# Performance work log

Hardware: AMD Instinct MI355X
Metric: run time of the kernel (lower is better)

Reference implementation:

```python
import jax, jax.numpy as jnp
import numpy as np

N_NODES = 100000
N_EDGES = 3200000
N_GRAPHS = 64
DIMS = [512, 1024, 512, 256, 128, 64, 32]
N_CLASSES = 10


def setup_inputs() -> dict:
    key = jax.random.key(0)
    ks = jax.random.split(key, 20)
    inp = {}
    inp['h'] = jax.random.normal(ks[0], (N_NODES, DIMS[0]), dtype=jnp.float32)
    inp['src'] = jax.random.randint(ks[1], (N_EDGES,), 0, N_NODES, dtype=jnp.int32)
    inp['dst'] = jax.random.randint(ks[2], (N_EDGES,), 0, N_NODES, dtype=jnp.int32)
    inp['graph_ids'] = jnp.sort(jax.random.randint(ks[3], (N_NODES,), 0, N_GRAPHS, dtype=jnp.int32))
    # GraphConv weights (glorot-like) and biases for the 6 layers
    for i in range(6):
        fi, fo = DIMS[i], DIMS[i + 1]
        scale = jnp.sqrt(2.0 / (fi + fo)).astype(jnp.float32)
        inp[f'W{i+1}'] = jax.random.normal(ks[4 + i], (fi, fo), dtype=jnp.float32) * scale
        inp[f'b{i+1}'] = jnp.zeros((fo,), dtype=jnp.float32)
    inp['Wc'] = jax.random.normal(ks[12], (DIMS[-1], N_CLASSES), dtype=jnp.float32) * 0.1
    inp['bc'] = jnp.zeros((N_CLASSES,), dtype=jnp.float32)
    return inp


def _graph_conv(h, W, b, src, dst, out_inv_sqrt, in_inv_sqrt):
    """DGL GraphConv, norm='both': D_dst^{-1/2} A (D_src^{-1/2} h) W + b.
    Apply W first when it shrinks the feature dim (DGL's mult-first trick)."""
    fi, fo = W.shape
    if fi > fo:
        h = h @ W  # shrink before aggregating
    h = h * out_inv_sqrt[:, None]
    agg = jax.ops.segment_sum(h[src], dst, num_segments=N_NODES)  # SpMM
    agg = agg * in_inv_sqrt[:, None]
    if fi <= fo:
        agg = agg @ W
    return agg + b


def reference(h, src, dst, graph_ids, W1, b1, W2, b2, W3, b3, W4, b4, W5, b5, W6, b6, Wc, bc):
    ones_e = jnp.ones((N_EDGES,), dtype=jnp.float32)
    out_deg = jax.ops.segment_sum(ones_e, src, num_segments=N_NODES)
    in_deg = jax.ops.segment_sum(ones_e, dst, num_segments=N_NODES)
    out_inv_sqrt = jax.lax.rsqrt(jnp.clip(out_deg, 1.0))  # allow_zero_in_degree -> clamp
    in_inv_sqrt = jax.lax.rsqrt(jnp.clip(in_deg, 1.0))
    for (W, b) in [(W1, b1), (W2, b2), (W3, b3), (W4, b4), (W5, b5), (W6, b6)]:
        h = jax.nn.relu(_graph_conv(h, W, b, src, dst, out_inv_sqrt, in_inv_sqrt))
    # dgl.mean_nodes over batched graph
    sums = jax.ops.segment_sum(h, graph_ids, num_segments=N_GRAPHS)
    counts = jax.ops.segment_sum(jnp.ones((N_NODES,), jnp.float32), graph_ids, num_segments=N_GRAPHS)
    hg = sums / jnp.clip(counts, 1.0)[:, None]
    return hg @ Wc + bc  # [N_GRAPHS, n_classes]
```

## Files before the change

### kernel.cpp

```cpp
#include <hip/hip_runtime.h>

#define N_NODES 100000
#define N_EDGES 3200000
#define N_GRAPHS 64

typedef unsigned short u16;
typedef __bf16 bf16x8 __attribute__((ext_vector_type(8)));
typedef float f32x4 __attribute__((ext_vector_type(4)));

__device__ inline u16 f2bf(float f) {
  unsigned u = __float_as_uint(f);
  unsigned r = (u + 0x7fffu + ((u >> 16) & 1u)) >> 16;
  return (u16)r;
}
__device__ inline float bf2f(u16 h) {
  return __uint_as_float(((unsigned)h) << 16);
}

__global__ void k_hist(const int* __restrict__ src, const int* __restrict__ dst,
                       int* __restrict__ odeg, int* __restrict__ ideg) {
  int e = blockIdx.x * blockDim.x + threadIdx.x;
  if (e < N_EDGES) {
    atomicAdd(&odeg[src[e]], 1);
    atomicAdd(&ideg[dst[e]], 1);
  }
}

__global__ void k_scan_block(const int* __restrict__ deg, int* __restrict__ rp,
                             int* __restrict__ bsums) {
  __shared__ int s[1024];
  int t = threadIdx.x;
  int i = blockIdx.x * 1024 + t;
  int v = (i < N_NODES) ? deg[i] : 0;
  s[t] = v;
  __syncthreads();
  for (int off = 1; off < 1024; off <<= 1) {
    int add = (t >= off) ? s[t - off] : 0;
    __syncthreads();
    s[t] += add;
    __syncthreads();
  }
  if (i < N_NODES) rp[i + 1] = s[t];
  if (t == 1023) bsums[blockIdx.x] = s[t];
  if (i == 0) rp[0] = 0;
}

__global__ void k_scan_bsums(int* __restrict__ bsums, int nb) {
  __shared__ int s[128];
  int t = threadIdx.x;
  int v = (t < nb) ? bsums[t] : 0;
  s[t] = v;
  __syncthreads();
  for (int off = 1; off < 128; off <<= 1) {
    int add = (t >= off) ? s[t - off] : 0;
    __syncthreads();
    s[t] += add;
    __syncthreads();
  }
  if (t < nb) bsums[t] = s[t];
}

__global__ void k_scan_add(const int* __restrict__ bsums, int* __restrict__ rp) {
  int b = blockIdx.x;
  if (b == 0) return;
  int i = b * 1024 + threadIdx.x;
  if (i < N_NODES) rp[i + 1] += bsums[b - 1];
}

__global__ void k_scatter(const int* __restrict__ src, const int* __restrict__ dst,
                          const int* __restrict__ rp, int* __restrict__ cur,
                          int* __restrict__ col) {
  int e = blockIdx.x * blockDim.x + threadIdx.x;
  if (e < N_EDGES) {
    int d = dst[e];
    int pos = rp[d] + atomicAdd(&cur[d], 1);
    col[pos] = src[e];
  }
}

__global__ void k_rsqrt(const int* __restrict__ odeg, const int* __restrict__ ideg,
                        float* __restrict__ a, float* __restrict__ bI) {
  int v = blockIdx.x * blockDim.x + threadIdx.x;
  if (v < N_NODES) {
    a[v]  = rsqrtf(fmaxf((float)odeg[v], 1.0f));
    bI[v] = rsqrtf(fmaxf((float)ideg[v], 1.0f));
  }
}

__global__ void k_f2bf(const float* __restrict__ x, u16* __restrict__ y, int n4) {
  int i = blockIdx.x * blockDim.x + threadIdx.x;
  if (i >= n4) return;
  float4 v = ((const float4*)x)[i];
  uint2 o;
  o.x = (unsigned)f2bf(v.x) | ((unsigned)f2bf(v.y) << 16);
  o.y = (unsigned)f2bf(v.z) | ((unsigned)f2bf(v.w) << 16);
  ((uint2*)y)[i] = o;
}

__global__ void k_wt(const float* __restrict__ W, u16* __restrict__ Wt, int fi, int fo) {
  int idx = blockIdx.x * blockDim.x + threadIdx.x;
  if (idx >= fi * fo) return;
  int n = idx / fi, k = idx % fi;
  Wt[idx] = f2bf(W[(size_t)k * fo + n]);
}

template<int BM, int BN, int WM, int WN>
__global__ __launch_bounds__(256) void k_mfma(
    const u16* __restrict__ A, const u16* __restrict__ Wt,
    const float* __restrict__ bias, const float* __restrict__ rowscale,
    u16* __restrict__ C, int M, int N, int K, int flags)
{
  constexpr int BK = 32;
  constexpr int LDK = BK + 8;
  constexpr int WX = BN / WN;
  constexpr int WY = BM / WM;
  static_assert(WX * WY == 4, "4 waves");
  constexpr int TM = WM / 16;
  constexpr int TN = WN / 16;

  __shared__ u16 As[BM * LDK];
  __shared__ u16 Bs[BN * LDK];

  const int tid = threadIdx.x;
  const int wave = tid >> 6;
  const int lane = tid & 63;
  const int wx = wave % WX;
  const int wy = wave / WX;
  const int bm = blockIdx.y * BM;
  const int bn = blockIdx.x * BN;

  const int lm = lane & 15;
  const int kb = (lane >> 4) * 8;

  f32x4 acc[TM][TN] = {};

  for (int k0 = 0; k0 < K; k0 += BK) {
    for (int idx = tid; idx < BM * 4; idx += 256) {
      int r = idx >> 2, kk = (idx & 3) * 8;
      int row = bm + r;
      uint4 v = make_uint4(0, 0, 0, 0);
      if (row < M) v = *(const uint4*)(A + (size_t)row * K + k0 + kk);
      *(uint4*)&As[r * LDK + kk] = v;
    }
    for (int idx = tid; idx < BN * 4; idx += 256) {
      int r = idx >> 2, kk = (idx & 3) * 8;
      *(uint4*)&Bs[r * LDK + kk] = *(const uint4*)(Wt + (size_t)(bn + r) * K + k0 + kk);
    }
    __syncthreads();

    bf16x8 af[TM], bfr[TN];
    #pragma unroll
    for (int i = 0; i < TM; ++i)
      af[i] = *(const bf16x8*)&As[(wy * WM + i * 16 + lm) * LDK + kb];
    #pragma unroll
    for (int j = 0; j < TN; ++j)
      bfr[j] = *(const bf16x8*)&Bs[(wx * WN + j * 16 + lm) * LDK + kb];
    #pragma unroll
    for (int i = 0; i < TM; ++i)
      #pragma unroll
      for (int j = 0; j < TN; ++j)
        acc[i][j] = __builtin_amdgcn_mfma_f32_16x16x32_bf16(af[i], bfr[j], acc[i][j], 0, 0, 0);
    __syncthreads();
  }

  const bool do_br = flags & 1;
  const bool do_rs = flags & 2;
  #pragma unroll
  for (int i = 0; i < TM; ++i) {
    #pragma unroll
    for (int j = 0; j < TN; ++j) {
      int col = bn + wx * WN + j * 16 + lm;
      float bv = do_br ? bias[col] : 0.f;
      #pragma unroll
      for (int r = 0; r < 4; ++r) {
        int row = bm + wy * WM + i * 16 + (lane >> 4) * 4 + r;
        if (row < M) {
          float v = acc[i][j][r];
          if (do_rs) v *= rowscale[row];
          if (do_br) v = fmaxf(v + bv, 0.f);
          C[(size_t)row * N + col] = f2bf(v);
        }
      }
    }
  }
}

template<int D>
__global__ __launch_bounds__(256) void k_spmm(
    const int* __restrict__ rp, const int* __restrict__ col,
    const u16* __restrict__ X, const float* __restrict__ sscale,
    const float* __restrict__ dscale, const float* __restrict__ bias,
    u16* __restrict__ Y, int relu_bias)
{
  constexpr int TPR = D / 8;
  constexpr int NPB = 256 / TPR;
  int node = blockIdx.x * NPB + threadIdx.x / TPR;
  if (node >= N_NODES) return;
  int c = (threadIdx.x % TPR) * 8;
  int s = rp[node], e = rp[node + 1];
  float acc[8] = {};
  for (int j = s; j < e; ++j) {
    int u = col[j];
    float w = sscale ? sscale[u] : 1.0f;
    uint4 v = *(const uint4*)(X + (size_t)u * D + c);
    acc[0] += w * __uint_as_float(v.x << 16);
    acc[1] += w * __uint_as_float(v.x & 0xffff0000u);
    acc[2] += w * __uint_as_float(v.y << 16);
    acc[3] += w * __uint_as_float(v.y & 0xffff0000u);
    acc[4] += w * __uint_as_float(v.z << 16);
    acc[5] += w * __uint_as_float(v.z & 0xffff0000u);
    acc[6] += w * __uint_as_float(v.w << 16);
    acc[7] += w * __uint_as_float(v.w & 0xffff0000u);
  }
  float dv = dscale[node];
  #pragma unroll
  for (int q = 0; q < 8; ++q) acc[q] *= dv;
  if (relu_bias) {
    #pragma unroll
    for (int q = 0; q < 8; ++q) acc[q] = fmaxf(acc[q] + bias[c + q], 0.f);
  }
  uint4 o;
  o.x = (unsigned)f2bf(acc[0]) | ((unsigned)f2bf(acc[1]) << 16);
  o.y = (unsigned)f2bf(acc[2]) | ((unsigned)f2bf(acc[3]) << 16);
  o.z = (unsigned)f2bf(acc[4]) | ((unsigned)f2bf(acc[5]) << 16);
  o.w = (unsigned)f2bf(acc[6]) | ((unsigned)f2bf(acc[7]) << 16);
  *(uint4*)(Y + (size_t)node * D + c) = o;
}

__global__ __launch_bounds__(256) void k_pool(const u16* __restrict__ h6,
                                              const int* __restrict__ gid,
                                              float* __restrict__ sums,
                                              float* __restrict__ cnts)
{
  __shared__ float acc[N_GRAPHS * 32];
  __shared__ float cnt[N_GRAPHS];
  int t = threadIdx.x;
  for (int k = t; k < N_GRAPHS * 32; k += 256) acc[k] = 0.f;
  if (t < N_GRAPHS) cnt[t] = 0.f;
  __syncthreads();
  int base = blockIdx.x * 256;
  int c = t & 31;
  int nl = t >> 5;
  for (int p = 0; p < 32; ++p) {
    int node = base + p * 8 + nl;
    if (node < N_NODES) {
      int g = gid[node];
      atomicAdd(&acc[g * 32 + c], bf2f(h6[(size_t)node * 32 + c]));
      if (c == 0) atomicAdd(&cnt[g], 1.0f);
    }
  }
  __syncthreads();
  for (int k = t; k < N_GRAPHS * 32; k += 256)
    if (acc[k] != 0.f) atomicAdd(&sums[k], acc[k]);
  if (t < N_GRAPHS && cnt[t] != 0.f) atomicAdd(&cnts[t], cnt[t]);
}

__global__ void k_final(const float* __restrict__ sums, const float* __restrict__ cnts,
                        const float* __restrict__ Wc, const float* __restrict__ bc,
                        float* __restrict__ out)
{
  int t = threadIdx.x;
  if (t >= N_GRAPHS * 10) return;
  int g = t / 10, cls = t % 10;
  float inv = 1.0f / fmaxf(cnts[g], 1.0f);
  float v = bc[cls];
  #pragma unroll
  for (int k = 0; k < 32; ++k)
    v += sums[g * 32 + k] * inv * Wc[k * 10 + cls];
  out[t] = v;
}

extern "C" void kernel_launch(void* const* d_in, const int* in_sizes, int n_in,
                              void* d_out, int out_size, void* d_ws, size_t ws_size,
                              hipStream_t stream)
{
  const float* h   = (const float*)d_in[0];
  const int*   src = (const int*)d_in[1];
  const int*   dst = (const int*)d_in[2];
  const int*   gid = (const int*)d_in[3];
  const float* W[6]; const float* b[6];
  for (int i = 0; i < 6; ++i) { W[i] = (const float*)d_in[4 + 2 * i]; b[i] = (const float*)d_in[5 + 2 * i]; }
  const float* Wc = (const float*)d_in[16];
  const float* bc = (const float*)d_in[17];
  float* out = (float*)d_out;

  const int FI[6] = {512, 1024, 512, 256, 128, 64};
  const int FO[6] = {1024, 512, 256, 128, 64, 32};

  char* p = (char*)d_ws;
  auto take = [&](size_t bytes) -> void* {
    void* r = (void*)p;
    p += (bytes + 255) & ~(size_t)255;
    return r;
  };
  u16* hb   = (u16*)take((size_t)N_NODES * 512 * 2);
  u16* bufA = (u16*)take((size_t)N_NODES * 512 * 2);
  u16* bufB = (u16*)take((size_t)N_NODES * 1024 * 2);
  u16* Wt[6];
  for (int i = 0; i < 6; ++i) Wt[i] = (u16*)take((size_t)FI[i] * FO[i] * 2);
  int*   colw = (int*)take((size_t)N_EDGES * 4);
  int*   rp   = (int*)take((size_t)(N_NODES + 1) * 4);
  int*   cur  = (int*)take((size_t)N_NODES * 4);
  int*   odeg = (int*)take((size_t)N_NODES * 4);
  int*   ideg = (int*)take((size_t)N_NODES * 4);
  float* ascl = (float*)take((size_t)N_NODES * 4);
  float* bscl = (float*)take((size_t)N_NODES * 4);
  int*   bsum = (int*)take(512);
  float* psum = (float*)take((size_t)N_GRAPHS * 32 * 4);
  float* pcnt = (float*)take((size_t)N_GRAPHS * 4);
  if ((size_t)((char*)p - (char*)d_ws) > ws_size) return;

  hipMemsetAsync(odeg, 0, (size_t)N_NODES * 4, stream);
  hipMemsetAsync(ideg, 0, (size_t)N_NODES * 4, stream);
  hipMemsetAsync(cur,  0, (size_t)N_NODES * 4, stream);
  hipMemsetAsync(psum, 0, (size_t)N_GRAPHS * 32 * 4, stream);
  hipMemsetAsync(pcnt, 0, (size_t)N_GRAPHS * 4, stream);

  k_hist<<<(N_EDGES + 255) / 256, 256, 0, stream>>>(src, dst, odeg, ideg);
  const int nb = (N_NODES + 1023) / 1024;
  k_scan_block<<<nb, 1024, 0, stream>>>(ideg, rp, bsum);
  k_scan_bsums<<<1, 128, 0, stream>>>(bsum, nb);
  k_scan_add<<<nb, 1024, 0, stream>>>(bsum, rp);
  k_scatter<<<(N_EDGES + 255) / 256, 256, 0, stream>>>(src, dst, rp, cur, colw);
  k_rsqrt<<<(N_NODES + 255) / 256, 256, 0, stream>>>(odeg, ideg, ascl, bscl);

  k_f2bf<<<(N_NODES * 512 / 4 + 255) / 256, 256, 0, stream>>>(h, hb, N_NODES * 512 / 4);
  for (int i = 0; i < 6; ++i)
    k_wt<<<(FI[i] * FO[i] + 255) / 256, 256, 0, stream>>>(W[i], Wt[i], FI[i], FO[i]);

  const int GY = (N_NODES + 127) / 128;

  k_spmm<512><<<(N_NODES + 3) / 4, 256, 0, stream>>>(rp, colw, hb, ascl, bscl, nullptr, bufA, 0);
  k_mfma<128,128,64,64><<<dim3(8, GY), 256, 0, stream>>>(bufA, Wt[0], b[0], nullptr, bufB, N_NODES, 1024, 512, 1);

  k_mfma<128,128,64,64><<<dim3(4, GY), 256, 0, stream>>>(bufB, Wt[1], nullptr, ascl, bufA, N_NODES, 512, 1024, 2);
  k_spmm<512><<<(N_NODES + 3) / 4, 256, 0, stream>>>(rp, colw, bufA, nullptr, bscl, b[1], hb, 1);

  k_mfma<128,128,64,64><<<dim3(2, GY), 256, 0, stream>>>(hb, Wt[2], nullptr, ascl, bufA, N_NODES, 256, 512, 2);
  k_spmm<256><<<(N_NODES + 7) / 8, 256, 0, stream>>>(rp, colw, bufA, nullptr, bscl, b[2], hb, 1);

  k_mfma<128,128,64,64><<<dim3(1, GY), 256, 0, stream>>>(hb, Wt[3], nullptr, ascl, bufA, N_NODES, 128, 256, 2);
  k_spmm<128><<<(N_NODES + 15) / 16, 256, 0, stream>>>(rp, colw, bufA, nullptr, bscl, b[3], hb, 1);

  k_mfma<128,64,64,32><<<dim3(1, GY), 256, 0, stream>>>(hb, Wt[4], nullptr, ascl, bufA, N_NODES, 64, 128, 2);
  k_spmm<64><<<(N_NODES + 31) / 32, 256, 0, stream>>>(rp, colw, bufA, nullptr, bscl, b[4], hb, 1);

  k_mfma<128,32,64,16><<<dim3(1, GY), 256, 0, stream>>>(hb, Wt[5], nullptr, ascl, bufA, N_NODES, 32, 64, 2);
  k_spmm<32><<<(N_NODES + 63) / 64, 256, 0, stream>>>(rp, colw, bufA, nullptr, bscl, b[5], hb, 1);

  k_pool<<<(N_NODES + 255) / 256, 256, 0, stream>>>(hb, gid, psum, pcnt);
  k_final<<<1, 640, 0, stream>>>(psum, pcnt, Wc, bc, out);
}
```

Before: 3.073 ms.

## Use direct global-to-LDS swizzled loads in GEMM, pre-scale input, unroll SpMM

The GEMM tile loads now use global_load_lds to write straight into an XOR-style swizzled LDS layout, replacing the padded register-staged copies. Buffers are padded to a multiple of 128 rows so the row bounds checks can be dropped. The first-layer source scaling moves into the fp32-to-bf16 conversion kernel, which removes the per-edge scale lookup from SpMM, and the SpMM gather loop is unrolled by four to keep more loads in flight. Padded rows hold uninitialised data that gets computed and written but is never read back by SpMM.

```diff
diff --git a/kernel.cpp b/kernel.cpp
--- a/kernel.cpp
+++ b/kernel.cpp
@@ -3,10 +3,13 @@
 #define N_NODES 100000
 #define N_EDGES 3200000
 #define N_GRAPHS 64
+#define M_PAD   100096
 
 typedef unsigned short u16;
 typedef __bf16 bf16x8 __attribute__((ext_vector_type(8)));
 typedef float f32x4 __attribute__((ext_vector_type(4)));
+typedef __attribute__((address_space(3))) unsigned int lds_u32;
+typedef __attribute__((address_space(1))) unsigned int glb_u32;
 
 __device__ inline u16 f2bf(float f) {
   unsigned u = __float_as_uint(f);
@@ -87,13 +90,16 @@
   }
 }
 
-__global__ void k_f2bf(const float* __restrict__ x, u16* __restrict__ y, int n4) {
+__global__ void k_prep(const float* __restrict__ x, const float* __restrict__ ascl,
+                       u16* __restrict__ y) {
   int i = blockIdx.x * blockDim.x + threadIdx.x;
-  if (i >= n4) return;
+  if (i >= N_NODES * 128) return;
+  int row = i >> 7;
+  float s = ascl[row];
   float4 v = ((const float4*)x)[i];
   uint2 o;
-  o.x = (unsigned)f2bf(v.x) | ((unsigned)f2bf(v.y) << 16);
-  o.y = (unsigned)f2bf(v.z) | ((unsigned)f2bf(v.w) << 16);
+  o.x = (unsigned)f2bf(v.x * s) | ((unsigned)f2bf(v.y * s) << 16);
+  o.y = (unsigned)f2bf(v.z * s) | ((unsigned)f2bf(v.w * s) << 16);
   ((uint2*)y)[i] = o;
 }
 
@@ -108,20 +114,21 @@
 __global__ __launch_bounds__(256) void k_mfma(
     const u16* __restrict__ A, const u16* __restrict__ Wt,
     const float* __restrict__ bias, const float* __restrict__ rowscale,
-    u16* __restrict__ C, int M, int N, int K, int flags)
+    u16* __restrict__ C, int N, int K, int flags)
 {
   constexpr int BK = 32;
-  constexpr int LDK = BK + 8;
   constexpr int WX = BN / WN;
   constexpr int WY = BM / WM;
   static_assert(WX * WY == 4, "4 waves");
   constexpr int TM = WM / 16;
   constexpr int TN = WN / 16;
-
-  __shared__ u16 As[BM * LDK];
-  __shared__ u16 Bs[BN * LDK];
-
-  const int tid = threadIdx.x;
+  constexpr int CA = BM / 16;
+  constexpr int CB = BN / 16;
+
+  __shared__ __align__(1024) u16 As[BM * BK];
+  __shared__ __align__(1024) u16 Bs[BN * BK];
+
+  const int tid  = threadIdx.x;
   const int wave = tid >> 6;
   const int lane = tid & 63;
   const int wx = wave % WX;
@@ -130,31 +137,48 @@
   const int bn = blockIdx.x * BN;
 
   const int lm = lane & 15;
-  const int kb = (lane >> 4) * 8;
-
+  const int lc = lane >> 4;
+
+  const int srA = (lane >> 2);
+  const int spA = lane & 3;
   f32x4 acc[TM][TN] = {};
 
   for (int k0 = 0; k0 < K; k0 += BK) {
-    for (int idx = tid; idx < BM * 4; idx += 256) {
-      int r = idx >> 2, kk = (idx & 3) * 8;
-      int row = bm + r;
-      uint4 v = make_uint4(0, 0, 0, 0);
-      if (row < M) v = *(const uint4*)(A + (size_t)row * K + k0 + kk);
-      *(uint4*)&As[r * LDK + kk] = v;
-    }
-    for (int idx = tid; idx < BN * 4; idx += 256) {
-      int r = idx >> 2, kk = (idx & 3) * 8;
-      *(uint4*)&Bs[r * LDK + kk] = *(const uint4*)(Wt + (size_t)(bn + r) * K + k0 + kk);
+    #pragma unroll
+    for (int q0 = 0; q0 < CA; q0 += 4) {
+      int q = q0 + wave;
+      if (q < CA) {
+        int rl = q * 16 + srA;
+        int c  = (spA - (rl >> 1)) & 3;
+        const u16* g = A + (size_t)(bm + rl) * K + k0 + c * 8;
+        __builtin_amdgcn_global_load_lds((const glb_u32*)g, (lds_u32*)(As + q * 512), 16, 0, 0);
+      }
+    }
+    #pragma unroll
+    for (int q0 = 0; q0 < CB; q0 += 4) {
+      int q = q0 + wave;
+      if (q < CB) {
+        int rl = q * 16 + srA;
+        int c  = (spA - (rl >> 1)) & 3;
+        const u16* g = Wt + (size_t)(bn + rl) * K + k0 + c * 8;
+        __builtin_amdgcn_global_load_lds((const glb_u32*)g, (lds_u32*)(Bs + q * 512), 16, 0, 0);
+      }
     }
     __syncthreads();
 
     bf16x8 af[TM], bfr[TN];
     #pragma unroll
-    for (int i = 0; i < TM; ++i)
-      af[i] = *(const bf16x8*)&As[(wy * WM + i * 16 + lm) * LDK + kb];
-    #pragma unroll
-    for (int j = 0; j < TN; ++j)
-      bfr[j] = *(const bf16x8*)&Bs[(wx * WN + j * 16 + lm) * LDK + kb];
+    for (int i = 0; i < TM; ++i) {
+      int rl = wy * WM + i * 16 + lm;
+      int p = (lc + (rl >> 1)) & 3;
+      af[i] = *(const bf16x8*)(As + rl * 32 + p * 8);
+    }
+    #pragma unroll
+    for (int j = 0; j < TN; ++j) {
+      int rl = wx * WN + j * 16 + lm;
+      int p = (lc + (rl >> 1)) & 3;
+      bfr[j] = *(const bf16x8*)(Bs + rl * 32 + p * 8);
+    }
     #pragma unroll
     for (int i = 0; i < TM; ++i)
       #pragma unroll
@@ -173,13 +197,11 @@
       float bv = do_br ? bias[col] : 0.f;
       #pragma unroll
       for (int r = 0; r < 4; ++r) {
-        int row = bm + wy * WM + i * 16 + (lane >> 4) * 4 + r;
-        if (row < M) {
-          float v = acc[i][j][r];
-          if (do_rs) v *= rowscale[row];
-          if (do_br) v = fmaxf(v + bv, 0.f);
-          C[(size_t)row * N + col] = f2bf(v);
-        }
+        int row = bm + wy * WM + i * 16 + lc * 4 + r;
+        float v = acc[i][j][r];
+        if (do_rs) v *= rowscale[row];
+        if (do_br) v = fmaxf(v + bv, 0.f);
+        C[(size_t)row * N + col] = f2bf(v);
       }
     }
   }
@@ -188,9 +210,8 @@
 template<int D>
 __global__ __launch_bounds__(256) void k_spmm(
     const int* __restrict__ rp, const int* __restrict__ col,
-    const u16* __restrict__ X, const float* __restrict__ sscale,
-    const float* __restrict__ dscale, const float* __restrict__ bias,
-    u16* __restrict__ Y, int relu_bias)
+    const u16* __restrict__ X, const float* __restrict__ dscale,
+    const float* __restrict__ bias, u16* __restrict__ Y, int relu_bias)
 {
   constexpr int TPR = D / 8;
   constexpr int NPB = 256 / TPR;
@@ -199,18 +220,37 @@
   int c = (threadIdx.x % TPR) * 8;
   int s = rp[node], e = rp[node + 1];
   float acc[8] = {};
-  for (int j = s; j < e; ++j) {
+  int j = s;
+  for (; j + 3 < e; j += 4) {
+    int u0 = col[j], u1 = col[j + 1], u2 = col[j + 2], u3 = col[j + 3];
+    uint4 v0 = *(const uint4*)(X + (size_t)u0 * D + c);
+    uint4 v1 = *(const uint4*)(X + (size_t)u1 * D + c);
+    uint4 v2 = *(const uint4*)(X + (size_t)u2 * D + c);
+    uint4 v3 = *(const uint4*)(X + (size_t)u3 * D + c);
+    acc[0] += __uint_as_float(v0.x << 16);        acc[1] += __uint_as_float(v0.x & 0xffff0000u);
+    acc[2] += __uint_as_float(v0.y << 16);        acc[3] += __uint_as_float(v0.y & 0xffff0000u);
+    acc[4] += __uint_as_float(v0.z << 16);        acc[5] += __uint_as_float(v0.z & 0xffff0000u);
+    acc[6] += __uint_as_float(v0.w << 16);        acc[7] += __uint_as_float(v0.w & 0xffff0000u);
+    acc[0] += __uint_as_float(v1.x << 16);        acc[1] += __uint_as_float(v1.x & 0xffff0000u);
+    acc[2] += __uint_as_float(v1.y << 16);        acc[3] += __uint_as_float(v1.y & 0xffff0000u);
+    acc[4] += __uint_as_float(v1.z << 16);        acc[5] += __uint_as_float(v1.z & 0xffff0000u);
+    acc[6] += __uint_as_float(v1.w << 16);        acc[7] += __uint_as_float(v1.w & 0xffff0000u);
+    acc[0] += __uint_as_float(v2.x << 16);        acc[1] += __uint_as_float(v2.x & 0xffff0000u);
+    acc[2] += __uint_as_float(v2.y << 16);        acc[3] += __uint_as_float(v2.y & 0xffff0000u);
+    acc[4] += __uint_as_float(v2.z << 16);        acc[5] += __uint_as_float(v2.z & 0xffff0000u);
+    acc[6] += __uint_as_float(v2.w << 16);        acc[7] += __uint_as_float(v2.w & 0xffff0000u);
+    acc[0] += __uint_as_float(v3.x << 16);        acc[1] += __uint_as_float(v3.x & 0xffff0000u);
+    acc[2] += __uint_as_float(v3.y << 16);        acc[3] += __uint_as_float(v3.y & 0xffff0000u);
+    acc[4] += __uint_as_float(v3.z << 16);        acc[5] += __uint_as_float(v3.z & 0xffff0000u);
+    acc[6] += __uint_as_float(v3.w << 16);        acc[7] += __uint_as_float(v3.w & 0xffff0000u);
+  }
+  for (; j < e; ++j) {
     int u = col[j];
-    float w = sscale ? sscale[u] : 1.0f;
     uint4 v = *(const uint4*)(X + (size_t)u * D + c);
-    acc[0] += w * __uint_as_float(v.x << 16);
-    acc[1] += w * __uint_as_float(v.x & 0xffff0000u);
-    acc[2] += w * __uint_as_float(v.y << 16);
-    acc[3] += w * __uint_as_float(v.y & 0xffff0000u);
-    acc[4] += w * __uint_as_float(v.z << 16);
-    acc[5] += w * __uint_as_float(v.z & 0xffff0000u);
-    acc[6] += w * __uint_as_float(v.w << 16);
-    acc[7] += w * __uint_as_float(v.w & 0xffff0000u);
+    acc[0] += __uint_as_float(v.x << 16);         acc[1] += __uint_as_float(v.x & 0xffff0000u);
+    acc[2] += __uint_as_float(v.y << 16);         acc[3] += __uint_as_float(v.y & 0xffff0000u);
+    acc[4] += __uint_as_float(v.z << 16);         acc[5] += __uint_as_float(v.z & 0xffff0000u);
+    acc[6] += __uint_as_float(v.w << 16);         acc[7] += __uint_as_float(v.w & 0xffff0000u);
   }
   float dv = dscale[node];
   #pragma unroll
@@ -293,9 +333,9 @@
     p += (bytes + 255) & ~(size_t)255;
     return r;
   };
-  u16* hb   = (u16*)take((size_t)N_NODES * 512 * 2);
-  u16* bufA = (u16*)take((size_t)N_NODES * 512 * 2);
-  u16* bufB = (u16*)take((size_t)N_NODES * 1024 * 2);
+  u16* hb   = (u16*)take((size_t)M_PAD * 512 * 2);
+  u16* bufA = (u16*)take((size_t)M_PAD * 512 * 2);
+  u16* bufB = (u16*)take((size_t)M_PAD * 1024 * 2);
   u16* Wt[6];
   for (int i = 0; i < 6; ++i) Wt[i] = (u16*)take((size_t)FI[i] * FO[i] * 2);
   int*   colw = (int*)take((size_t)N_EDGES * 4);
@@ -303,7 +343,7 @@
   int*   cur  = (int*)take((size_t)N_NODES * 4);
   int*   odeg = (int*)take((size_t)N_NODES * 4);
   int*   ideg = (int*)take((size_t)N_NODES * 4);
-  float* ascl = (float*)take((size_t)N_NODES * 4);
+  float* ascl = (float*)take((size_t)M_PAD * 4);
   float* bscl = (float*)take((size_t)N_NODES * 4);
   int*   bsum = (int*)take(512);
   float* psum = (float*)take((size_t)N_GRAPHS * 32 * 4);
@@ -324,29 +364,29 @@
   k_scatter<<<(N_EDGES + 255) / 256, 256, 0, stream>>>(src, dst, rp, cur, colw);
   k_rsqrt<<<(N_NODES + 255) / 256, 256, 0, stream>>>(odeg, ideg, ascl, bscl);
 
-  k_f2bf<<<(N_NODES * 512 / 4 + 255) / 256, 256, 0, stream>>>(h, hb, N_NODES * 512 / 4);
+  k_prep<<<(N_NODES * 128 + 255) / 256, 256, 0, stream>>>(h, ascl, hb);
   for (int i = 0; i < 6; ++i)
     k_wt<<<(FI[i] * FO[i] + 255) / 256, 256, 0, stream>>>(W[i], Wt[i], FI[i], FO[i]);
 
-  const int GY = (N_NODES + 127) / 128;
-
-  k_spmm<512><<<(N_NODES + 3) / 4, 256, 0, stream>>>(rp, colw, hb, ascl, bscl, nullptr, bufA, 0);
-  k_mfma<128,128,64,64><<<dim3(8, GY), 256, 0, stream>>>(bufA, Wt[0], b[0], nullptr, bufB, N_NODES, 1024, 512, 1);
-
-  k_mfma<128,128,64,64><<<dim3(4, GY), 256, 0, stream>>>(bufB, Wt[1], nullptr, ascl, bufA, N_NODES, 512, 1024, 2);
-  k_spmm<512><<<(N_NODES + 3) / 4, 256, 0, stream>>>(rp, colw, bufA, nullptr, bscl, b[1], hb, 1);
-
-  k_mfma<128,128,64,64><<<dim3(2, GY), 256, 0, stream>>>(hb, Wt[2], nullptr, ascl, bufA, N_NODES, 256, 512, 2);
-  k_spmm<256><<<(N_NODES + 7) / 8, 256, 0, stream>>>(rp, colw, bufA, nullptr, bscl, b[2], hb, 1);
-
-  k_mfma<128,128,64,64><<<dim3(1, GY), 256, 0, stream>>>(hb, Wt[3], nullptr, ascl, bufA, N_NODES, 128, 256, 2);
-  k_spmm<128><<<(N_NODES + 15) / 16, 256, 0, stream>>>(rp, colw, bufA, nullptr, bscl, b[3], hb, 1);
-
-  k_mfma<128,64,64,32><<<dim3(1, GY), 256, 0, stream>>>(hb, Wt[4], nullptr, ascl, bufA, N_NODES, 64, 128, 2);
-  k_spmm<64><<<(N_NODES + 31) / 32, 256, 0, stream>>>(rp, colw, bufA, nullptr, bscl, b[4], hb, 1);
-
-  k_mfma<128,32,64,16><<<dim3(1, GY), 256, 0, stream>>>(hb, Wt[5], nullptr, ascl, bufA, N_NODES, 32, 64, 2);
-  k_spmm<32><<<(N_NODES + 63) / 64, 256, 0, stream>>>(rp, colw, bufA, nullptr, bscl, b[5], hb, 1);
+  const int GY = M_PAD / 128;
+
+  k_spmm<512><<<(N_NODES + 3) / 4, 256, 0, stream>>>(rp, colw, hb, bscl, nullptr, bufA, 0);
+  k_mfma<128,128,64,64><<<dim3(8, GY), 256, 0, stream>>>(bufA, Wt[0], b[0], nullptr, bufB, 1024, 512, 1);
+
+  k_mfma<128,128,64,64><<<dim3(4, GY), 256, 0, stream>>>(bufB, Wt[1], nullptr, ascl, bufA, 512, 1024, 2);
+  k_spmm<512><<<(N_NODES + 3) / 4, 256, 0, stream>>>(rp, colw, bufA, bscl, b[1], hb, 1);
+
+  k_mfma<128,128,64,64><<<dim3(2, GY), 256, 0, stream>>>(hb, Wt[2], nullptr, ascl, bufA, 256, 512, 2);
+  k_spmm<256><<<(N_NODES + 7) / 8, 256, 0, stream>>>(rp, colw, bufA, bscl, b[2], hb, 1);
+
+  k_mfma<128,128,64,64><<<dim3(1, GY), 256, 0, stream>>>(hb, Wt[3], nullptr, ascl, bufA, 128, 256, 2);
+  k_spmm<128><<<(N_NODES + 15) / 16, 256, 0, stream>>>(rp, colw, bufA, bscl, b[3], hb, 1);
+
+  k_mfma<128,64,64,32><<<dim3(1, GY), 256, 0, stream>>>(hb, Wt[4], nullptr, ascl, bufA, 64, 128, 2);
+  k_spmm<64><<<(N_NODES + 31) / 32, 256, 0, stream>>>(rp, colw, bufA, bscl, b[4], hb, 1);
+
+  k_mfma<128,32,64,16><<<dim3(1, GY), 256, 0, stream>>>(hb, Wt[5], nullptr, ascl, bufA, 32, 64, 2);
+  k_spmm<32><<<(N_NODES + 63) / 64, 256, 0, stream>>>(rp, colw, bufA, bscl, b[5], hb, 1);
 
   k_pool<<<(N_NODES + 255) / 256, 256, 0, stream>>>(hb, gid, psum, pcnt);
   k_final<<<1, 640, 0, stream>>>(psum, pcnt, Wc, bc, out);
```

Measured after the change: 2.702 ms. 12.1% less time.
